# Optimization experiments

Hardware: AMD Instinct MI355X
Metric: run time of the kernel (lower is better)

The kernel has to match this reference:

```python
import jax, jax.numpy as jnp
import numpy as np
import math

B, S, F, R = 16, 2048, 512, 4
EPS = 1e-5

def setup_inputs() -> dict:
    key = jax.random.key(0)
    ks = jax.random.split(key, 8)
    s = 1.0 / math.sqrt(S)
    return {
        "x": jax.random.normal(ks[0], (B, S, F), dtype=jnp.float32),
        "Wq": jax.random.uniform(ks[1], (R, S), jnp.float32, -s, s),
        "bq": jnp.zeros((R,), jnp.float32),
        "Wk": jax.random.uniform(ks[2], (R, S), jnp.float32, -s, s),
        "bk": jnp.zeros((R,), jnp.float32),
        "Wv": jax.random.uniform(ks[3], (S, S), jnp.float32, -s, s),
        "bv": jnp.zeros((S,), jnp.float32),
        "ln_w": jnp.ones((S, F), jnp.float32),
        "ln_b": jnp.zeros((S, F), jnp.float32),
        "alpha": jnp.asarray(0.1, jnp.float32),
        "beta": jnp.asarray(0.1, jnp.float32),
    }

def reference(x, Wq, bq, Wk, bk, Wv, bv, ln_w, ln_b, alpha, beta):
    # LayerNorm over last two dims [S, F]
    mu = jnp.mean(x, axis=(1, 2), keepdims=True)
    var = jnp.mean(jnp.square(x - mu), axis=(1, 2), keepdims=True)
    x_norm = (x - mu) * jax.lax.rsqrt(var + EPS) * ln_w + ln_b
    x_t = jnp.swapaxes(x_norm, 1, 2)  # [B, F, S]
    Q = jnp.einsum('bfs,rs->bfr', x_t, Wq) + bq  # [B, F, R]
    K = jnp.einsum('bfs,rs->bfr', x_t, Wk) + bk  # [B, F, R]
    A = jnp.einsum('bfr,bgr->bfg', Q, K) / math.sqrt(R)  # [B, F, F]
    A = jax.nn.softmax(A, axis=-1)
    V = jnp.einsum('bfs,ts->bft', x_t, Wv) + bv  # [B, F, S]
    out = jnp.einsum('bfg,bgs->bfs', A, V)  # [B, F, S]
    # dropout in eval mode = identity
    out = x_t + alpha * out + V + beta * V
    return jnp.swapaxes(out, 1, 2)  # [B, S, F]
```

## Files before the change

kernel.cpp:

```cpp
#include <hip/hip_runtime.h>
#include <hip/hip_bf16.h>

#define NB 16
#define SS 2048
#define FF 512

typedef __bf16 bf16_t;
typedef __bf16 bf16x8 __attribute__((ext_vector_type(8)));
typedef __bf16 bf16x4 __attribute__((ext_vector_type(4)));
typedef float  f32x4  __attribute__((ext_vector_type(4)));

__global__ __launch_bounds__(64) void zero_stats(float* sums) {
    if (threadIdx.x < 32) sums[threadIdx.x] = 0.0f;
}

__global__ __launch_bounds__(256) void stats_kernel(const float* __restrict__ x,
                                                    float* __restrict__ sums) {
    const int b = blockIdx.y;
    const float* xb = x + ((size_t)b << 20) + (size_t)blockIdx.x * 16384;
    float s = 0.0f, ss = 0.0f;
#pragma unroll
    for (int i = 0; i < 16; ++i) {
        const float4 v = *(const float4*)&xb[(threadIdx.x + i * 256) * 4];
        s  += v.x + v.y + v.z + v.w;
        ss += v.x * v.x + v.y * v.y + v.z * v.z + v.w * v.w;
    }
#pragma unroll
    for (int off = 32; off > 0; off >>= 1) {
        s  += __shfl_down(s, off);
        ss += __shfl_down(ss, off);
    }
    __shared__ float ps[4], pss[4];
    const int w = threadIdx.x >> 6, lane = threadIdx.x & 63;
    if (lane == 0) { ps[w] = s; pss[w] = ss; }
    __syncthreads();
    if (threadIdx.x == 0) {
        atomicAdd(&sums[b],      ps[0] + ps[1] + ps[2] + ps[3]);
        atomicAdd(&sums[16 + b], pss[0] + pss[1] + pss[2] + pss[3]);
    }
}

__global__ __launch_bounds__(64) void finalize_stats(const float* __restrict__ sums,
                                                     float* __restrict__ musig) {
    const int b = threadIdx.x;
    if (b < 16) {
        const float inv_n = 1.0f / 1048576.0f;
        const float mu  = sums[b] * inv_n;
        const float var = sums[16 + b] * inv_n - mu * mu;
        musig[b]      = mu;
        musig[16 + b] = rsqrtf(var + 1e-5f);
    }
}

__global__ __launch_bounds__(256) void ynorm_kernel(const float* __restrict__ x,
                                                    const float* __restrict__ lw,
                                                    const float* __restrict__ lb,
                                                    const float* __restrict__ musig,
                                                    bf16_t* __restrict__ Y) {
    __shared__ bf16_t t[32][33];
    const int b = blockIdx.z;
    const int f0 = blockIdx.x * 32, s0 = blockIdx.y * 32;
    const float mu = musig[b], rs = musig[16 + b];
    const int c = threadIdx.x & 31, rb = threadIdx.x >> 5;
#pragma unroll
    for (int i = 0; i < 4; ++i) {
        const int s_loc = rb + i * 8;
        const size_t idx = (size_t)(s0 + s_loc) * FF + f0 + c;
        const float yv = (x[((size_t)b << 20) + idx] - mu) * rs * lw[idx] + lb[idx];
        t[s_loc][c] = (bf16_t)yv;
    }
    __syncthreads();
#pragma unroll
    for (int i = 0; i < 4; ++i) {
        const int f_loc = rb + i * 8;
        Y[((size_t)b << 20) + (size_t)(f0 + f_loc) * SS + s0 + c] = t[c][f_loc];
    }
}

__global__ __launch_bounds__(256) void cast_wv(const float* __restrict__ Wv,
                                               bf16_t* __restrict__ Wvb) {
    const size_t i = ((size_t)blockIdx.x * 256 + threadIdx.x) * 4;
    const float4 v = *(const float4*)&Wv[i];
    bf16x4 o;
    o[0] = (bf16_t)v.x; o[1] = (bf16_t)v.y; o[2] = (bf16_t)v.z; o[3] = (bf16_t)v.w;
    *(bf16x4*)&Wvb[i] = o;
}

__global__ __launch_bounds__(256) void qk_kernel(const bf16_t* __restrict__ Y,
                                                 const float* __restrict__ Wq,
                                                 const float* __restrict__ bq,
                                                 const float* __restrict__ Wk,
                                                 const float* __restrict__ bk,
                                                 float* __restrict__ Qo,
                                                 float* __restrict__ Ko) {
    const int w = threadIdx.x >> 6, lane = threadIdx.x & 63;
    const int row = blockIdx.x * 4 + w;
    const bf16_t* y = Y + (size_t)row * SS;
    float qa[4] = {0.f, 0.f, 0.f, 0.f}, ka[4] = {0.f, 0.f, 0.f, 0.f};
#pragma unroll
    for (int c = 0; c < 4; ++c) {
        const int s = c * 512 + lane * 8;
        const bf16x8 yv = *(const bf16x8*)&y[s];
        float yf[8];
#pragma unroll
        for (int j = 0; j < 8; ++j) yf[j] = (float)yv[j];
#pragma unroll
        for (int r = 0; r < 4; ++r) {
            const float4 a0 = *(const float4*)&Wq[r * SS + s];
            const float4 a1 = *(const float4*)&Wq[r * SS + s + 4];
            const float4 c0 = *(const float4*)&Wk[r * SS + s];
            const float4 c1 = *(const float4*)&Wk[r * SS + s + 4];
            qa[r] += yf[0]*a0.x + yf[1]*a0.y + yf[2]*a0.z + yf[3]*a0.w
                   + yf[4]*a1.x + yf[5]*a1.y + yf[6]*a1.z + yf[7]*a1.w;
            ka[r] += yf[0]*c0.x + yf[1]*c0.y + yf[2]*c0.z + yf[3]*c0.w
                   + yf[4]*c1.x + yf[5]*c1.y + yf[6]*c1.z + yf[7]*c1.w;
        }
    }
#pragma unroll
    for (int off = 32; off > 0; off >>= 1) {
#pragma unroll
        for (int r = 0; r < 4; ++r) {
            qa[r] += __shfl_down(qa[r], off);
            ka[r] += __shfl_down(ka[r], off);
        }
    }
    if (lane == 0) {
#pragma unroll
        for (int r = 0; r < 4; ++r) {
            Qo[(size_t)row * 4 + r] = qa[r] + bq[r];
            Ko[(size_t)row * 4 + r] = ka[r] + bk[r];
        }
    }
}

__global__ __launch_bounds__(256) void softmax_kernel(const float* __restrict__ Qo,
                                                      const float* __restrict__ Ko,
                                                      bf16_t* __restrict__ Aout) {
    const int w = threadIdx.x >> 6, lane = threadIdx.x & 63;
    const int row = blockIdx.x * 4 + w;
    const int b = row >> 9;
    const float4 q = *(const float4*)&Qo[(size_t)row * 4];
    const float* kb = Ko + (size_t)b * FF * 4;
    float sc[8];
#pragma unroll
    for (int j = 0; j < 8; ++j) {
        const float4 kv = *(const float4*)&kb[(lane * 8 + j) * 4];
        sc[j] = (q.x*kv.x + q.y*kv.y + q.z*kv.z + q.w*kv.w) * 0.5f;
    }
    float mx = sc[0];
#pragma unroll
    for (int j = 1; j < 8; ++j) mx = fmaxf(mx, sc[j]);
#pragma unroll
    for (int off = 32; off > 0; off >>= 1) mx = fmaxf(mx, __shfl_xor(mx, off));
    float sum = 0.f;
#pragma unroll
    for (int j = 0; j < 8; ++j) { sc[j] = __expf(sc[j] - mx); sum += sc[j]; }
#pragma unroll
    for (int off = 32; off > 0; off >>= 1) sum += __shfl_xor(sum, off);
    const float inv = 1.0f / sum;
    bf16x8 o;
#pragma unroll
    for (int j = 0; j < 8; ++j) o[j] = (bf16_t)(sc[j] * inv);
    *(bf16x8*)&Aout[(size_t)row * FF + lane * 8] = o;
}

__global__ __launch_bounds__(512, 2) void gemm_nt_8phase(
        const bf16_t* __restrict__ Abase, long long strideA, int lda,
        const bf16_t* __restrict__ Bbase, long long strideB, int ldb,
        bf16_t* __restrict__ Cbase, long long strideC, int ldc,
        int NTILES, const float* __restrict__ bias_m) {
    __shared__ __align__(16) bf16_t As[2][16384];
    __shared__ __align__(16) bf16_t Bs[2][16384];
    const int tid = threadIdx.x;
    const int w = tid >> 6, lane = tid & 63;
    const int m0 = blockIdx.x * 256, n0 = blockIdx.y * 256;
    const bf16_t* A = Abase + (size_t)blockIdx.z * (size_t)strideA;
    const bf16_t* B = Bbase + (size_t)blockIdx.z * (size_t)strideB;
    bf16_t* C = Cbase + (size_t)blockIdx.z * (size_t)strideC;
    const int wm = w >> 2, wn = w & 3;

    const int rr0 = (w * 2 + 0) * 16 + (lane >> 2);
    const int rr1 = (w * 2 + 1) * 16 + (lane >> 2);
    const int sw0 = ((lane & 3) ^ ((rr0 >> 1) & 3)) * 8;
    const int sw1 = ((lane & 3) ^ ((rr1 >> 1) & 3)) * 8;
    const bf16_t* gA0 = A + (size_t)(m0 + rr0) * lda + sw0;
    const bf16_t* gA1 = A + (size_t)(m0 + rr1) * lda + sw1;
    const bf16_t* gB0 = B + (size_t)(n0 + rr0) * ldb + sw0;
    const bf16_t* gB1 = B + (size_t)(n0 + rr1) * ldb + sw1;
    const int d0 = (w * 2 + 0) * 512;
    const int d1 = (w * 2 + 1) * 512;

#define STA(bi, h, ko) do {                                                          \
    __builtin_amdgcn_global_load_lds(                                                \
        (const __attribute__((address_space(1))) unsigned int*)(gA0 + (ko) + (h)*32),\
        (__attribute__((address_space(3))) unsigned int*)&As[bi][(h)*8192 + d0], 16, 0, 0); \
    __builtin_amdgcn_global_load_lds(                                                \
        (const __attribute__((address_space(1))) unsigned int*)(gA1 + (ko) + (h)*32),\
        (__attribute__((address_space(3))) unsigned int*)&As[bi][(h)*8192 + d1], 16, 0, 0); \
} while (0)
#define STB(bi, h, ko) do {                                                          \
    __builtin_amdgcn_global_load_lds(                                                \
        (const __attribute__((address_space(1))) unsigned int*)(gB0 + (ko) + (h)*32),\
        (__attribute__((address_space(3))) unsigned int*)&Bs[bi][(h)*8192 + d0], 16, 0, 0); \
    __builtin_amdgcn_global_load_lds(                                                \
        (const __attribute__((address_space(1))) unsigned int*)(gB1 + (ko) + (h)*32),\
        (__attribute__((address_space(3))) unsigned int*)&Bs[bi][(h)*8192 + d1], 16, 0, 0); \
} while (0)

    const int cs = lane >> 4;
    int offA[2][8], offB[2][4];
#pragma unroll
    for (int kk = 0; kk < 2; ++kk) {
#pragma unroll
        for (int mt = 0; mt < 8; ++mt) {
            const int r = wm * 128 + mt * 16 + (lane & 15);
            offA[kk][mt] = kk * 8192 + r * 32 + ((cs ^ ((r >> 1) & 3)) << 3);
        }
#pragma unroll
        for (int nt = 0; nt < 4; ++nt) {
            const int r = wn * 64 + nt * 16 + (lane & 15);
            offB[kk][nt] = kk * 8192 + r * 32 + ((cs ^ ((r >> 1) & 3)) << 3);
        }
    }

#define DS_A(kk, mh) do { _Pragma("unroll")                                   \
    for (int i = 0; i < 4; ++i) af[i] = *(const bf16x8*)&as[offA[kk][(mh)*4 + i]]; } while (0)
#define DS_B(kk) do { _Pragma("unroll")                                       \
    for (int i = 0; i < 4; ++i) bfr[i] = *(const bf16x8*)&bs[offB[kk][i]]; } while (0)
#define MFMA16(mh) do { _Pragma("unroll")                                     \
    for (int i = 0; i < 4; ++i) { _Pragma("unroll")                           \
        for (int nt = 0; nt < 4; ++nt)                                        \
            acc[(mh)*4 + i][nt] = __builtin_amdgcn_mfma_f32_16x16x32_bf16(    \
                af[i], bfr[nt], acc[(mh)*4 + i][nt], 0, 0, 0); } } while (0)
#define WAITB asm volatile("s_waitcnt vmcnt(4)\n\ts_barrier" ::: "memory")
#define LGKM0 do { asm volatile("s_waitcnt lgkmcnt(0)" ::: "memory");         \
                   __builtin_amdgcn_sched_barrier(0); } while (0)
#define SBAR  __builtin_amdgcn_sched_barrier(0)

    f32x4 acc[8][4] = {};
    const int mask = NTILES - 1;

    STA(0, 0, 0); STB(0, 0, 0); STA(0, 1, 0); STB(0, 1, 0);

    for (int t = 0; t < NTILES; ++t) {
        const int cur = t & 1, oth = cur ^ 1;
        const int ko = ((t + 1) & mask) * 64;
        const bf16_t* as = As[cur];
        const bf16_t* bs = Bs[cur];
        bf16x8 af[4], bfr[4];
        WAITB;
        DS_A(0, 0); DS_B(0); SBAR; STA(oth, 0, ko); LGKM0;
        __builtin_amdgcn_s_setprio(1); MFMA16(0); __builtin_amdgcn_s_setprio(0); SBAR;
        DS_A(0, 1); SBAR; STB(oth, 0, ko); LGKM0;
        __builtin_amdgcn_s_setprio(1); MFMA16(1); __builtin_amdgcn_s_setprio(0); SBAR;
        WAITB;
        DS_A(1, 0); DS_B(1); SBAR; STA(oth, 1, ko); LGKM0;
        __builtin_amdgcn_s_setprio(1); MFMA16(0); __builtin_amdgcn_s_setprio(0); SBAR;
        DS_A(1, 1); SBAR; STB(oth, 1, ko); LGKM0;
        __builtin_amdgcn_s_setprio(1); MFMA16(1); __builtin_amdgcn_s_setprio(0); SBAR;
    }
#undef STA
#undef STB
#undef DS_A
#undef DS_B
#undef MFMA16
#undef WAITB
#undef LGKM0
#undef SBAR

#pragma unroll
    for (int mt = 0; mt < 8; ++mt) {
#pragma unroll
        for (int r = 0; r < 4; ++r) {
            const int row = m0 + wm * 128 + mt * 16 + ((lane >> 4) << 2) + r;
            const float bm = bias_m ? bias_m[row] : 0.0f;
#pragma unroll
            for (int nt = 0; nt < 4; ++nt) {
                const int col = n0 + wn * 64 + nt * 16 + (lane & 15);
                C[(size_t)row * ldc + col] = (bf16_t)(acc[mt][nt][r] + bm);
            }
        }
    }
}

__global__ __launch_bounds__(256) void epilogue_kernel(const float* __restrict__ x,
                                                       const float* __restrict__ lw,
                                                       const float* __restrict__ lb,
                                                       const bf16_t* __restrict__ Ot,
                                                       const bf16_t* __restrict__ Vt,
                                                       const float* __restrict__ musig,
                                                       const float* __restrict__ alphap,
                                                       const float* __restrict__ betap,
                                                       float* __restrict__ out) {
    const size_t i4 = ((size_t)blockIdx.x * 256 + threadIdx.x) * 4;
    const size_t b = i4 >> 20;
    const size_t rr = i4 & 1048575;
    const float mu = musig[b], rs = musig[16 + b];
    const float alpha = alphap[0];
    const float onepb = 1.0f + betap[0];
    const float4 xv  = *(const float4*)&x[i4];
    const float4 wv  = *(const float4*)&lw[rr];
    const float4 bbv = *(const float4*)&lb[rr];
    const bf16x4 ov = *(const bf16x4*)&Ot[i4];
    const bf16x4 vv = *(const bf16x4*)&Vt[i4];
    float4 o;
    o.x = (xv.x - mu) * rs * wv.x + bbv.x + alpha * (float)ov[0] + onepb * (float)vv[0];
    o.y = (xv.y - mu) * rs * wv.y + bbv.y + alpha * (float)ov[1] + onepb * (float)vv[1];
    o.z = (xv.z - mu) * rs * wv.z + bbv.z + alpha * (float)ov[2] + onepb * (float)vv[2];
    o.w = (xv.w - mu) * rs * wv.w + bbv.w + alpha * (float)ov[3] + onepb * (float)vv[3];
    *(float4*)&out[i4] = o;
}

extern "C" void kernel_launch(void* const* d_in, const int* in_sizes, int n_in,
                              void* d_out, int out_size, void* d_ws, size_t ws_size,
                              hipStream_t stream) {
    const float* x   = (const float*)d_in[0];
    const float* Wq  = (const float*)d_in[1];
    const float* bq  = (const float*)d_in[2];
    const float* Wk  = (const float*)d_in[3];
    const float* bk  = (const float*)d_in[4];
    const float* Wv  = (const float*)d_in[5];
    const float* bv  = (const float*)d_in[6];
    const float* lw  = (const float*)d_in[7];
    const float* lb  = (const float*)d_in[8];
    const float* alp = (const float*)d_in[9];
    const float* bet = (const float*)d_in[10];
    float* out = (float*)d_out;

    char* ws = (char*)d_ws;
    float*  sums  = (float*)(ws + 0);
    float*  musig = (float*)(ws + 128);
    float*  Qo    = (float*)(ws + 256);
    float*  Ko    = (float*)(ws + 256 + 131072);
    bf16_t* Wvb   = (bf16_t*)(ws + 262400);
    bf16_t* Asm   = (bf16_t*)(ws + 8651008);
    bf16_t* Vt    = (bf16_t*)(ws + 17039616);
    bf16_t* Y     = (bf16_t*)(ws + 50594048);
    bf16_t* Ot    = Y;

    zero_stats<<<1, 64, 0, stream>>>(sums);
    stats_kernel<<<dim3(64, 16), 256, 0, stream>>>(x, sums);
    finalize_stats<<<1, 64, 0, stream>>>(sums, musig);
    cast_wv<<<4096, 256, 0, stream>>>(Wv, Wvb);
    ynorm_kernel<<<dim3(16, 64, 16), 256, 0, stream>>>(x, lw, lb, musig, Y);
    qk_kernel<<<2048, 256, 0, stream>>>(Y, Wq, bq, Wk, bk, Qo, Ko);
    softmax_kernel<<<2048, 256, 0, stream>>>(Qo, Ko, Asm);
    gemm_nt_8phase<<<dim3(8, 2, 16), 512, 0, stream>>>(
        Wvb, 0, SS, Y, 1 << 20, SS, Vt, 1 << 20, FF, 32, bv);
    gemm_nt_8phase<<<dim3(8, 2, 16), 512, 0, stream>>>(
        Vt, 1 << 20, FF, Asm, FF * FF, FF, Ot, 1 << 20, FF, 8, nullptr);
    epilogue_kernel<<<16384, 256, 0, stream>>>(x, lw, lb, Ot, Vt, musig, alp, bet, out);
}
```

Before: 213.4 us.

## Remap GEMM blocks across XCDs, add ping-pong barriers, drop stats atomics

The GEMM now launches as a flat 1D grid of 256 blocks. Each block ID is remapped so that the blocks sharing a batch land on the same XCD (blockIdx & 7 chunking), which should improve L2 reuse. The main loop's barrier placement changes: s_barrier calls now wrap each MFMA cluster and the vmcnt waits are split out, giving a ping-pong-style schedule between the two waves per SIMD. The LayerNorm statistics switch from atomics to per-block partials reduced in a 256-thread finalize kernel, which removes the zeroing kernel but reuses the Asm workspace region for the partials. The extra barriers could add synchronisation stalls.

```diff
diff --git a/kernel.cpp b/kernel.cpp
--- a/kernel.cpp
+++ b/kernel.cpp
@@ -10,12 +10,8 @@
 typedef __bf16 bf16x4 __attribute__((ext_vector_type(4)));
 typedef float  f32x4  __attribute__((ext_vector_type(4)));
 
-__global__ __launch_bounds__(64) void zero_stats(float* sums) {
-    if (threadIdx.x < 32) sums[threadIdx.x] = 0.0f;
-}
-
 __global__ __launch_bounds__(256) void stats_kernel(const float* __restrict__ x,
-                                                    float* __restrict__ sums) {
+                                                    float* __restrict__ partials) {
     const int b = blockIdx.y;
     const float* xb = x + ((size_t)b << 20) + (size_t)blockIdx.x * 16384;
     float s = 0.0f, ss = 0.0f;
@@ -35,18 +31,30 @@
     if (lane == 0) { ps[w] = s; pss[w] = ss; }
     __syncthreads();
     if (threadIdx.x == 0) {
-        atomicAdd(&sums[b],      ps[0] + ps[1] + ps[2] + ps[3]);
-        atomicAdd(&sums[16 + b], pss[0] + pss[1] + pss[2] + pss[3]);
-    }
-}
-
-__global__ __launch_bounds__(64) void finalize_stats(const float* __restrict__ sums,
-                                                     float* __restrict__ musig) {
-    const int b = threadIdx.x;
-    if (b < 16) {
+        partials[b * 64 + blockIdx.x]        = ps[0] + ps[1] + ps[2] + ps[3];
+        partials[1024 + b * 64 + blockIdx.x] = pss[0] + pss[1] + pss[2] + pss[3];
+    }
+}
+
+__global__ __launch_bounds__(256) void finalize_stats(const float* __restrict__ partials,
+                                                      float* __restrict__ musig) {
+    const int tid = threadIdx.x;
+    const int b = tid >> 4, i = tid & 15;
+    float s = 0.f, ss = 0.f;
+#pragma unroll
+    for (int j = 0; j < 4; ++j) {
+        s  += partials[b * 64 + i * 4 + j];
+        ss += partials[1024 + b * 64 + i * 4 + j];
+    }
+#pragma unroll
+    for (int off = 8; off > 0; off >>= 1) {
+        s  += __shfl_xor(s, off);
+        ss += __shfl_xor(ss, off);
+    }
+    if (i == 0) {
         const float inv_n = 1.0f / 1048576.0f;
-        const float mu  = sums[b] * inv_n;
-        const float var = sums[16 + b] * inv_n - mu * mu;
+        const float mu  = s * inv_n;
+        const float var = ss * inv_n - mu * mu;
         musig[b]      = mu;
         musig[16 + b] = rsqrtf(var + 1e-5f);
     }
@@ -173,10 +181,16 @@
     __shared__ __align__(16) bf16_t Bs[2][16384];
     const int tid = threadIdx.x;
     const int w = tid >> 6, lane = tid & 63;
-    const int m0 = blockIdx.x * 256, n0 = blockIdx.y * 256;
-    const bf16_t* A = Abase + (size_t)blockIdx.z * (size_t)strideA;
-    const bf16_t* B = Bbase + (size_t)blockIdx.z * (size_t)strideB;
-    bf16_t* C = Cbase + (size_t)blockIdx.z * (size_t)strideC;
+
+    const int nchunk = gridDim.x >> 3;
+    const int wgid = (blockIdx.x & 7) * nchunk + (blockIdx.x >> 3);
+    const int bz = wgid >> 4;
+    const int rem = wgid & 15;
+    const int m0 = (rem & 7) * 256, n0 = (rem >> 3) * 256;
+
+    const bf16_t* A = Abase + (size_t)bz * (size_t)strideA;
+    const bf16_t* B = Bbase + (size_t)bz * (size_t)strideB;
+    bf16_t* C = Cbase + (size_t)bz * (size_t)strideC;
     const int wm = w >> 2, wn = w & 3;
 
     const int rr0 = (w * 2 + 0) * 16 + (lane >> 2);
@@ -232,41 +246,64 @@
         for (int nt = 0; nt < 4; ++nt)                                        \
             acc[(mh)*4 + i][nt] = __builtin_amdgcn_mfma_f32_16x16x32_bf16(    \
                 af[i], bfr[nt], acc[(mh)*4 + i][nt], 0, 0, 0); } } while (0)
-#define WAITB asm volatile("s_waitcnt vmcnt(4)\n\ts_barrier" ::: "memory")
+#define VM4   asm volatile("s_waitcnt vmcnt(4)" ::: "memory")
+#define HBAR  __builtin_amdgcn_s_barrier()
 #define LGKM0 do { asm volatile("s_waitcnt lgkmcnt(0)" ::: "memory");         \
                    __builtin_amdgcn_sched_barrier(0); } while (0)
 #define SBAR  __builtin_amdgcn_sched_barrier(0)
+#define PRIO1 __builtin_amdgcn_s_setprio(1)
+#define PRIO0 __builtin_amdgcn_s_setprio(0)
 
     f32x4 acc[8][4] = {};
     const int mask = NTILES - 1;
 
     STA(0, 0, 0); STB(0, 0, 0); STA(0, 1, 0); STB(0, 1, 0);
+    VM4; HBAR;
 
     for (int t = 0; t < NTILES; ++t) {
-        const int cur = t & 1, oth = cur ^ 1;
+        const int oth = (t & 1) ^ 1;
         const int ko = ((t + 1) & mask) * 64;
-        const bf16_t* as = As[cur];
-        const bf16_t* bs = Bs[cur];
+        const bf16_t* as = As[t & 1];
+        const bf16_t* bs = Bs[t & 1];
         bf16x8 af[4], bfr[4];
-        WAITB;
-        DS_A(0, 0); DS_B(0); SBAR; STA(oth, 0, ko); LGKM0;
-        __builtin_amdgcn_s_setprio(1); MFMA16(0); __builtin_amdgcn_s_setprio(0); SBAR;
-        DS_A(0, 1); SBAR; STB(oth, 0, ko); LGKM0;
-        __builtin_amdgcn_s_setprio(1); MFMA16(1); __builtin_amdgcn_s_setprio(0); SBAR;
-        WAITB;
-        DS_A(1, 0); DS_B(1); SBAR; STA(oth, 1, ko); LGKM0;
-        __builtin_amdgcn_s_setprio(1); MFMA16(0); __builtin_amdgcn_s_setprio(0); SBAR;
-        DS_A(1, 1); SBAR; STB(oth, 1, ko); LGKM0;
-        __builtin_amdgcn_s_setprio(1); MFMA16(1); __builtin_amdgcn_s_setprio(0); SBAR;
+        DS_A(0, 0); DS_B(0); SBAR;
+        STA(oth, 0, ko); SBAR;
+        HBAR;
+        LGKM0;
+        PRIO1; MFMA16(0); PRIO0; SBAR;
+        HBAR;
+        DS_A(0, 1); SBAR;
+        STB(oth, 0, ko); SBAR;
+        VM4;
+        HBAR;
+        LGKM0;
+        PRIO1; MFMA16(1); PRIO0; SBAR;
+        HBAR;
+        DS_A(1, 0); DS_B(1); SBAR;
+        STA(oth, 1, ko); SBAR;
+        HBAR;
+        LGKM0;
+        PRIO1; MFMA16(0); PRIO0; SBAR;
+        HBAR;
+        DS_A(1, 1); SBAR;
+        STB(oth, 1, ko); SBAR;
+        VM4;
+        HBAR;
+        LGKM0;
+        PRIO1; MFMA16(1); PRIO0; SBAR;
+        HBAR;
     }
 #undef STA
 #undef STB
 #undef DS_A
 #undef DS_B
 #undef MFMA16
-#undef WAITB
+#undef VM4
+#undef HBAR
 #undef LGKM0
 #undef SBAR
+#undef PRIO1
+#undef PRIO0
 
 #pragma unroll
     for (int mt = 0; mt < 8; ++mt) {
@@ -328,26 +365,25 @@
     float* out = (float*)d_out;
 
     char* ws = (char*)d_ws;
-    float*  sums  = (float*)(ws + 0);
     float*  musig = (float*)(ws + 128);
     float*  Qo    = (float*)(ws + 256);
     float*  Ko    = (float*)(ws + 256 + 131072);
     bf16_t* Wvb   = (bf16_t*)(ws + 262400);
     bf16_t* Asm   = (bf16_t*)(ws + 8651008);
+    float*  partials = (float*)(ws + 8651008);
     bf16_t* Vt    = (bf16_t*)(ws + 17039616);
     bf16_t* Y     = (bf16_t*)(ws + 50594048);
     bf16_t* Ot    = Y;
 
-    zero_stats<<<1, 64, 0, stream>>>(sums);
-    stats_kernel<<<dim3(64, 16), 256, 0, stream>>>(x, sums);
-    finalize_stats<<<1, 64, 0, stream>>>(sums, musig);
+    stats_kernel<<<dim3(64, 16), 256, 0, stream>>>(x, partials);
+    finalize_stats<<<1, 256, 0, stream>>>(partials, musig);
     cast_wv<<<4096, 256, 0, stream>>>(Wv, Wvb);
     ynorm_kernel<<<dim3(16, 64, 16), 256, 0, stream>>>(x, lw, lb, musig, Y);
     qk_kernel<<<2048, 256, 0, stream>>>(Y, Wq, bq, Wk, bk, Qo, Ko);
     softmax_kernel<<<2048, 256, 0, stream>>>(Qo, Ko, Asm);
-    gemm_nt_8phase<<<dim3(8, 2, 16), 512, 0, stream>>>(
+    gemm_nt_8phase<<<256, 512, 0, stream>>>(
         Wvb, 0, SS, Y, 1 << 20, SS, Vt, 1 << 20, FF, 32, bv);
-    gemm_nt_8phase<<<dim3(8, 2, 16), 512, 0, stream>>>(
+    gemm_nt_8phase<<<256, 512, 0, stream>>>(
         Vt, 1 << 20, FF, Asm, FF * FF, FF, Ot, 1 << 20, FF, 8, nullptr);
     epilogue_kernel<<<16384, 256, 0, stream>>>(x, lw, lb, Ot, Vt, musig, alp, bet, out);
 }
```

Measured after the change: 195.1 us. 8.6% less time.
